# Kernel tuning notes

Measured on AMD Instinct MI355X. Metric: run time of the kernel, lower is better.

Reference implementation:

```python
import jax, jax.numpy as jnp
import numpy as np

S, T, D, H, DQ, F = 2048, 2048, 1024, 16, 1024, 4096
HD = DQ // H


def _layernorm(x, w, b, eps=1e-5):
    mu = jnp.mean(x, axis=-1, keepdims=True)
    var = jnp.mean((x - mu) ** 2, axis=-1, keepdims=True)
    return (x - mu) / jnp.sqrt(var + eps) * w + b


def _attention(q_in, kv_in, mask, wq, bq, wk, bk, wv, bv, wo, bo):
    # q_in: [Sq, D], kv_in: [Sk, D]
    q = (q_in @ wq + bq).reshape(-1, H, HD).transpose(1, 0, 2)   # [H, Sq, hd]
    k = (kv_in @ wk + bk).reshape(-1, H, HD).transpose(1, 0, 2)  # [H, Sk, hd]
    v = (kv_in @ wv + bv).reshape(-1, H, HD).transpose(1, 0, 2)
    scale = jnp.sqrt(jnp.asarray(HD, dtype=q.dtype))
    scores = jnp.einsum('hqd,hkd->hqk', q, k) / scale            # [H, Sq, Sk]
    if mask is not None:
        scores = jnp.where(mask, scores, jnp.finfo(scores.dtype).min)
    attn = jax.nn.softmax(scores, axis=-1)
    ctx = jnp.einsum('hqk,hkd->hqd', attn, v)                    # [H, Sq, hd]
    ctx = ctx.transpose(1, 0, 2).reshape(-1, H * HD)             # [Sq, DQ]
    return ctx @ wo + bo


def setup_inputs() -> dict:
    key = jax.random.key(0)
    ks = jax.random.split(key, 20)

    def lin(kk, fan_in, shape):
        return jax.random.normal(kk, shape, dtype=jnp.float32) / np.sqrt(fan_in)

    inp = {
        'inputs': jax.random.normal(ks[0], (S, D), dtype=jnp.float32),
        'encoder_outputs': jax.random.normal(ks[1], (T, D), dtype=jnp.float32),
        'self_attention_mask': jnp.tril(jnp.ones((S, S), dtype=bool)),
        'cross_attention_mask': jnp.ones((S, T), dtype=bool),
        'ln1_w': jnp.ones((D,), jnp.float32), 'ln1_b': jnp.zeros((D,), jnp.float32),
        'ln2_w': jnp.ones((D,), jnp.float32), 'ln2_b': jnp.zeros((D,), jnp.float32),
        'ln3_w': jnp.ones((D,), jnp.float32), 'ln3_b': jnp.zeros((D,), jnp.float32),
        'sa_wq': lin(ks[2], D, (D, DQ)), 'sa_bq': jnp.zeros((DQ,), jnp.float32),
        'sa_wk': lin(ks[3], D, (D, DQ)), 'sa_bk': jnp.zeros((DQ,), jnp.float32),
        'sa_wv': lin(ks[4], D, (D, DQ)), 'sa_bv': jnp.zeros((DQ,), jnp.float32),
        'sa_wo': lin(ks[5], DQ, (DQ, D)), 'sa_bo': jnp.zeros((D,), jnp.float32),
        'ca_wq': lin(ks[6], D, (D, DQ)), 'ca_bq': jnp.zeros((DQ,), jnp.float32),
        'ca_wk': lin(ks[7], D, (D, DQ)), 'ca_bk': jnp.zeros((DQ,), jnp.float32),
        'ca_wv': lin(ks[8], D, (D, DQ)), 'ca_bv': jnp.zeros((DQ,), jnp.float32),
        'ca_wo': lin(ks[9], DQ, (DQ, D)), 'ca_bo': jnp.zeros((D,), jnp.float32),
        'mlp_wi': lin(ks[10], D, (D, F)), 'mlp_bi': jnp.zeros((F,), jnp.float32),
        'mlp_wo': lin(ks[11], F, (F, D)), 'mlp_bo': jnp.zeros((D,), jnp.float32),
    }
    return inp


def reference(inputs, encoder_outputs, self_attention_mask, cross_attention_mask,
              ln1_w, ln1_b, ln2_w, ln2_b, ln3_w, ln3_b,
              sa_wq, sa_bq, sa_wk, sa_bk, sa_wv, sa_bv, sa_wo, sa_bo,
              ca_wq, ca_bq, ca_wk, ca_bk, ca_wv, ca_bv, ca_wo, ca_bo,
              mlp_wi, mlp_bi, mlp_wo, mlp_bo):
    # pre-norm self-attention
    n1 = _layernorm(inputs, ln1_w, ln1_b)
    x = inputs + _attention(n1, n1, self_attention_mask,
                            sa_wq, sa_bq, sa_wk, sa_bk, sa_wv, sa_bv, sa_wo, sa_bo)
    # pre-norm cross-attention (kv from encoder, not normalized)
    n2 = _layernorm(x, ln2_w, ln2_b)
    x = x + _attention(n2, encoder_outputs, cross_attention_mask,
                       ca_wq, ca_bq, ca_wk, ca_bk, ca_wv, ca_bv, ca_wo, ca_bo)
    # pre-norm MLP
    n3 = _layernorm(x, ln3_w, ln3_b)
    h = jax.nn.relu(n3 @ mlp_wi + mlp_bi)
    return x + (h @ mlp_wo + mlp_bo)
```

## Files before the change

kernel.cpp:

```cpp
#include <hip/hip_runtime.h>


#define S_LEN 2048
#define T_LEN 2048
#define D_DIM 1024
#define H_NUM 16
#define DQ_DIM 1024
#define F_DIM 4096
#define HD_DIM 64

typedef _Float16 f16x8 __attribute__((ext_vector_type(8)));
typedef _Float16 f16x4 __attribute__((ext_vector_type(4)));
typedef float f32x4 __attribute__((ext_vector_type(4)));

__device__ __forceinline__ void split1(float x, _Float16& h, _Float16& l) {
    _Float16 hh = (_Float16)x;
    h = hh;
    l = (_Float16)((x - (float)hh) * 2048.0f);
}

struct WC8 { const float* w[8]; _Float16* th[8]; _Float16* tl[8]; };

__global__ __launch_bounds__(256)
void wconv_kernel(WC8 a, int K, int N) {
    __shared__ __align__(16) _Float16 th[64][72], tl[64][72];
    const float* W = a.w[blockIdx.z];
    _Float16* Th = a.th[blockIdx.z];
    _Float16* Tl = a.tl[blockIdx.z];
    int n0 = blockIdx.x * 64, k0 = blockIdx.y * 64;
    int t = threadIdx.x;
#pragma unroll
    for (int i = 0; i < 4; ++i) {
        int idx = i * 256 + t;
        int kk = idx >> 4, nq = idx & 15;
        float4 w4 = *(const float4*)(W + (size_t)(k0 + kk) * N + n0 + nq * 4);
        _Float16 h, l;
        split1(w4.x, h, l); th[nq * 4 + 0][kk] = h; tl[nq * 4 + 0][kk] = l;
        split1(w4.y, h, l); th[nq * 4 + 1][kk] = h; tl[nq * 4 + 1][kk] = l;
        split1(w4.z, h, l); th[nq * 4 + 2][kk] = h; tl[nq * 4 + 2][kk] = l;
        split1(w4.w, h, l); th[nq * 4 + 3][kk] = h; tl[nq * 4 + 3][kk] = l;
    }
    __syncthreads();
#pragma unroll
    for (int i = 0; i < 2; ++i) {
        int idx = i * 256 + t;
        int nn = idx >> 3, kq = idx & 7;
        *(f16x8*)(Th + (size_t)(n0 + nn) * K + k0 + kq * 8) = *(const f16x8*)&th[nn][kq * 8];
        *(f16x8*)(Tl + (size_t)(n0 + nn) * K + k0 + kq * 8) = *(const f16x8*)&tl[nn][kq * 8];
    }
}

__global__ __launch_bounds__(256)
void esplit_kernel(const float* __restrict__ x, _Float16* __restrict__ hi,
                   _Float16* __restrict__ lo) {
    size_t i = ((size_t)blockIdx.x * 256 + threadIdx.x) * 4;
    float4 v = *(const float4*)(x + i);
    f16x4 hv, lv; _Float16 h, l;
    split1(v.x, h, l); hv[0] = h; lv[0] = l;
    split1(v.y, h, l); hv[1] = h; lv[1] = l;
    split1(v.z, h, l); hv[2] = h; lv[2] = l;
    split1(v.w, h, l); hv[3] = h; lv[3] = l;
    *(f16x4*)(hi + i) = hv;
    *(f16x4*)(lo + i) = lv;
}

__global__ __launch_bounds__(256)
void ln_kernel(const float* __restrict__ x, const float* __restrict__ w,
               const float* __restrict__ b, _Float16* __restrict__ outh,
               _Float16* __restrict__ outl) {
    int row = blockIdx.x;
    int t = threadIdx.x;
    float4 v = ((const float4*)(x + (size_t)row * D_DIM))[t];
    float s = v.x + v.y + v.z + v.w;
    float ss = v.x * v.x + v.y * v.y + v.z * v.z + v.w * v.w;
#pragma unroll
    for (int m = 1; m < 64; m <<= 1) {
        s += __shfl_xor(s, m, 64);
        ss += __shfl_xor(ss, m, 64);
    }
    __shared__ float ps[4], pss[4];
    int wid = t >> 6;
    if ((t & 63) == 0) { ps[wid] = s; pss[wid] = ss; }
    __syncthreads();
    s = ps[0] + ps[1] + ps[2] + ps[3];
    ss = pss[0] + pss[1] + pss[2] + pss[3];
    float mu = s * (1.0f / D_DIM);
    float var = ss * (1.0f / D_DIM) - mu * mu;
    float rstd = rsqrtf(var + 1e-5f);
    float4 wv = ((const float4*)w)[t];
    float4 bv = ((const float4*)b)[t];
    f16x4 hv, lv; _Float16 h, l;
    split1((v.x - mu) * rstd * wv.x + bv.x, h, l); hv[0] = h; lv[0] = l;
    split1((v.y - mu) * rstd * wv.y + bv.y, h, l); hv[1] = h; lv[1] = l;
    split1((v.z - mu) * rstd * wv.z + bv.z, h, l); hv[2] = h; lv[2] = l;
    split1((v.w - mu) * rstd * wv.w + bv.w, h, l); hv[3] = h; lv[3] = l;
    *(f16x4*)(outh + (size_t)row * D_DIM + t * 4) = hv;
    *(f16x4*)(outl + (size_t)row * D_DIM + t * 4) = lv;
}

struct GemmArgs {
    const _Float16 *Ah[3], *Al[3];
    const _Float16 *Bh[3], *Bl[3];
    const float *bias[3];
    void *C0[3];
    void *C1[3];
};

template <int EPI, int BM>
__global__ __launch_bounds__(256, 2)
void gemm_kernel(GemmArgs ga, int M, int N, int K) {
    static_assert(BM == 64 || BM == 128, "BM");
    constexpr int MI = BM / 32;
    constexpr int CA = BM / 32;
    int z = blockIdx.z;
    const _Float16* Ap[2] = {ga.Ah[z], ga.Al[z]};
    const _Float16* Bp[2] = {ga.Bh[z], ga.Bl[z]};
    const float* bias = ga.bias[z];
    void* C0 = ga.C0[z];
    void* C1 = ga.C1[z];

    __shared__ __align__(16) _Float16 sA[2][BM][64];
    __shared__ __align__(16) _Float16 sB[2][64][64];

    int t = threadIdx.x;
    int m0 = blockIdx.y * BM, n0 = blockIdx.x * 64;
    int lane = t & 63, wid = t >> 6;
    int g = lane >> 4, l15 = lane & 15;
    int wm = wid >> 1, wn = wid & 1;

    f32x4 acc1[MI][2] = {};
    f32x4 acc2[MI][2] = {};

    f16x8 ra[2][CA], rb[2][2];
    const int nt = K / 64;

#pragma unroll
    for (int p = 0; p < 2; ++p) {
#pragma unroll
        for (int i = 0; i < CA; ++i) {
            int id = i * 256 + t, row = id >> 3, c = id & 7;
            ra[p][i] = *(const f16x8*)(Ap[p] + (size_t)(m0 + row) * K + c * 8);
        }
#pragma unroll
        for (int i = 0; i < 2; ++i) {
            int id = i * 256 + t, row = id >> 3, c = id & 7;
            rb[p][i] = *(const f16x8*)(Bp[p] + (size_t)(n0 + row) * K + c * 8);
        }
    }

    for (int kt = 0; kt < nt; ++kt) {
        __syncthreads();
#pragma unroll
        for (int p = 0; p < 2; ++p) {
#pragma unroll
            for (int i = 0; i < CA; ++i) {
                int id = i * 256 + t, row = id >> 3, c = id & 7;
                *(f16x8*)&sA[p][row][(c ^ (row & 7)) * 8] = ra[p][i];
            }
#pragma unroll
            for (int i = 0; i < 2; ++i) {
                int id = i * 256 + t, row = id >> 3, c = id & 7;
                *(f16x8*)&sB[p][row][(c ^ (row & 7)) * 8] = rb[p][i];
            }
        }
        if (kt + 1 < nt) {
            int k0 = (kt + 1) * 64;
#pragma unroll
            for (int p = 0; p < 2; ++p) {
#pragma unroll
                for (int i = 0; i < CA; ++i) {
                    int id = i * 256 + t, row = id >> 3, c = id & 7;
                    ra[p][i] = *(const f16x8*)(Ap[p] + (size_t)(m0 + row) * K + k0 + c * 8);
                }
#pragma unroll
                for (int i = 0; i < 2; ++i) {
                    int id = i * 256 + t, row = id >> 3, c = id & 7;
                    rb[p][i] = *(const f16x8*)(Bp[p] + (size_t)(n0 + row) * K + k0 + c * 8);
                }
            }
        }
        __syncthreads();
#pragma unroll
        for (int ks = 0; ks < 2; ++ks) {
            f16x8 ah[MI], al[MI], bh[2], bl[2];
#pragma unroll
            for (int mi = 0; mi < MI; ++mi) {
                int row = wm * (BM / 2) + mi * 16 + l15;
                int cc = ((ks * 4 + g) ^ (row & 7)) * 8;
                ah[mi] = *(const f16x8*)&sA[0][row][cc];
                al[mi] = *(const f16x8*)&sA[1][row][cc];
            }
#pragma unroll
            for (int ni = 0; ni < 2; ++ni) {
                int row = wn * 32 + ni * 16 + l15;
                int cc = ((ks * 4 + g) ^ (row & 7)) * 8;
                bh[ni] = *(const f16x8*)&sB[0][row][cc];
                bl[ni] = *(const f16x8*)&sB[1][row][cc];
            }
#pragma unroll
            for (int mi = 0; mi < MI; ++mi)
#pragma unroll
                for (int ni = 0; ni < 2; ++ni) {
                    acc1[mi][ni] = __builtin_amdgcn_mfma_f32_16x16x32_f16(ah[mi], bh[ni], acc1[mi][ni], 0, 0, 0);
                    acc2[mi][ni] = __builtin_amdgcn_mfma_f32_16x16x32_f16(ah[mi], bl[ni], acc2[mi][ni], 0, 0, 0);
                    acc2[mi][ni] = __builtin_amdgcn_mfma_f32_16x16x32_f16(al[mi], bh[ni], acc2[mi][ni], 0, 0, 0);
                }
        }
    }

#pragma unroll
    for (int ni = 0; ni < 2; ++ni) {
        int col = n0 + wn * 32 + ni * 16 + l15;
        float bb = bias[col];
#pragma unroll
        for (int mi = 0; mi < MI; ++mi) {
#pragma unroll
            for (int r = 0; r < 4; ++r) {
                int row = m0 + wm * (BM / 2) + mi * 16 + g * 4 + r;
                float v = acc1[mi][ni][r] + acc2[mi][ni][r] * (1.0f / 2048.0f) + bb;
                size_t off = (size_t)row * N + col;
                if constexpr (EPI == 0) {
                    ((_Float16*)C0)[off] = (_Float16)v;
                } else if constexpr (EPI == 1) {
                    ((float*)C0)[off] = v + ((const float*)C1)[off];
                } else {
                    _Float16 h, l;
                    split1(fmaxf(v, 0.0f), h, l);
                    ((_Float16*)C0)[off] = h;
                    ((_Float16*)C1)[off] = l;
                }
            }
        }
    }
}

template <bool CAUSAL>
__global__ __launch_bounds__(256)
void flash_kernel(const _Float16* __restrict__ Qm, const _Float16* __restrict__ Km,
                  const _Float16* __restrict__ Vm, _Float16* __restrict__ Oh,
                  _Float16* __restrict__ Ol, int Sk) {
    __shared__ __align__(16) _Float16 sK[64][72];
    __shared__ __align__(16) _Float16 sV[64][72];
    __shared__ __align__(16) _Float16 sP[4][16][72];

    int t = threadIdx.x, lane = t & 63, wid = t >> 6;
    int g = lane >> 4, l15 = lane & 15;
    int qt = blockIdx.x, h = blockIdx.y;
    int q0w = qt * 64 + wid * 16;

    f16x8 aq[2];
    {
        const _Float16* qp = Qm + (size_t)(q0w + l15) * DQ_DIM + h * HD_DIM;
#pragma unroll
        for (int ks = 0; ks < 2; ++ks) {
            f16x8 a = *(const f16x8*)(qp + ks * 32 + g * 8);
#pragma unroll
            for (int e = 0; e < 8; ++e) a[e] = a[e] * (_Float16)0.125f;
            aq[ks] = a;
        }
    }

    float m_old[4] = {-1e30f, -1e30f, -1e30f, -1e30f};
    float l_run[4] = {0.f, 0.f, 0.f, 0.f};
    f32x4 o[4] = {};

    int ntiles = CAUSAL ? (qt + 1) : (Sk / 64);
    for (int jt = 0; jt < ntiles; ++jt) {
        int j0 = jt * 64;
        __syncthreads();
#pragma unroll
        for (int i = 0; i < 2; ++i) {
            int idx = i * 256 + t;
            int jj = idx >> 3, dq = idx & 7;
            *(f16x8*)&sK[jj][dq * 8] =
                *(const f16x8*)(Km + (size_t)(j0 + jj) * DQ_DIM + h * HD_DIM + dq * 8);
            f16x8 v8 = *(const f16x8*)(Vm + (size_t)(j0 + jj) * DQ_DIM + h * HD_DIM + dq * 8);
#pragma unroll
            for (int e = 0; e < 8; ++e) sV[dq * 8 + e][jj] = v8[e];
        }
        __syncthreads();

        f32x4 sc[4] = {};
#pragma unroll
        for (int cf = 0; cf < 4; ++cf)
#pragma unroll
            for (int ks = 0; ks < 2; ++ks) {
                f16x8 bk = *(const f16x8*)&sK[cf * 16 + l15][ks * 32 + g * 8];
                sc[cf] = __builtin_amdgcn_mfma_f32_16x16x32_f16(aq[ks], bk, sc[cf], 0, 0, 0);
            }
        if (CAUSAL && jt == qt) {
#pragma unroll
            for (int cf = 0; cf < 4; ++cf)
#pragma unroll
                for (int r = 0; r < 4; ++r)
                    if (j0 + cf * 16 + l15 > q0w + g * 4 + r) sc[cf][r] = -1e30f;
        }

#pragma unroll
        for (int r = 0; r < 4; ++r) {
            float tmax = fmaxf(fmaxf(sc[0][r], sc[1][r]), fmaxf(sc[2][r], sc[3][r]));
#pragma unroll
            for (int mm = 1; mm < 16; mm <<= 1) tmax = fmaxf(tmax, __shfl_xor(tmax, mm, 64));
            float mn = fmaxf(m_old[r], tmax);
            float corr = __expf(m_old[r] - mn);
            float rs = 0.0f;
#pragma unroll
            for (int cf = 0; cf < 4; ++cf) {
                float p = __expf(sc[cf][r] - mn);
                sc[cf][r] = p;
                rs += p;
            }
#pragma unroll
            for (int mm = 1; mm < 16; mm <<= 1) rs += __shfl_xor(rs, mm, 64);
            l_run[r] = l_run[r] * corr + rs;
            m_old[r] = mn;
#pragma unroll
            for (int hf = 0; hf < 4; ++hf) o[hf][r] *= corr;
        }

#pragma unroll
        for (int cf = 0; cf < 4; ++cf)
#pragma unroll
            for (int r = 0; r < 4; ++r)
                sP[wid][g * 4 + r][cf * 16 + l15] = (_Float16)sc[cf][r];
        __syncthreads();
#pragma unroll
        for (int ks = 0; ks < 2; ++ks) {
            f16x8 ap = *(const f16x8*)&sP[wid][l15][ks * 32 + g * 8];
#pragma unroll
            for (int hf = 0; hf < 4; ++hf) {
                f16x8 bv = *(const f16x8*)&sV[hf * 16 + l15][ks * 32 + g * 8];
                o[hf] = __builtin_amdgcn_mfma_f32_16x16x32_f16(ap, bv, o[hf], 0, 0, 0);
            }
        }
    }

#pragma unroll
    for (int hf = 0; hf < 4; ++hf)
#pragma unroll
        for (int r = 0; r < 4; ++r) {
            int row = q0w + g * 4 + r;
            int col = h * HD_DIM + hf * 16 + l15;
            _Float16 hh, ll;
            split1(o[hf][r] / l_run[r], hh, ll);
            Oh[(size_t)row * DQ_DIM + col] = hh;
            Ol[(size_t)row * DQ_DIM + col] = ll;
        }
}

#define MB(x) ((size_t)(x) * 1024 * 1024)

extern "C" void kernel_launch(void* const* d_in, const int* in_sizes, int n_in,
                              void* d_out, int out_size, void* d_ws, size_t ws_size,
                              hipStream_t stream) {
    const float* x_in = (const float*)d_in[0];
    const float* enc  = (const float*)d_in[1];
    const float* ln1w = (const float*)d_in[4];  const float* ln1b = (const float*)d_in[5];
    const float* ln2w = (const float*)d_in[6];  const float* ln2b = (const float*)d_in[7];
    const float* ln3w = (const float*)d_in[8];  const float* ln3b = (const float*)d_in[9];
    const float* sa_wq = (const float*)d_in[10]; const float* sa_bq = (const float*)d_in[11];
    const float* sa_wk = (const float*)d_in[12]; const float* sa_bk = (const float*)d_in[13];
    const float* sa_wv = (const float*)d_in[14]; const float* sa_bv = (const float*)d_in[15];
    const float* sa_wo = (const float*)d_in[16]; const float* sa_bo = (const float*)d_in[17];
    const float* ca_wq = (const float*)d_in[18]; const float* ca_bq = (const float*)d_in[19];
    const float* ca_wk = (const float*)d_in[20]; const float* ca_bk = (const float*)d_in[21];
    const float* ca_wv = (const float*)d_in[22]; const float* ca_bv = (const float*)d_in[23];
    const float* ca_wo = (const float*)d_in[24]; const float* ca_bo = (const float*)d_in[25];
    const float* mlp_wi = (const float*)d_in[26]; const float* mlp_bi = (const float*)d_in[27];
    const float* mlp_wo = (const float*)d_in[28]; const float* mlp_bo = (const float*)d_in[29];
    float* out = (float*)d_out;

    char* base = (char*)d_ws;
    float* X        = (float*)(base + MB(0));
    _Float16* Nbh   = (_Float16*)(base + MB(8));
    _Float16* Nbl   = (_Float16*)(base + MB(12));
    _Float16* Qb    = (_Float16*)(base + MB(16));
    _Float16* Kb    = (_Float16*)(base + MB(20));
    _Float16* Vb    = (_Float16*)(base + MB(24));
    _Float16* CXh   = (_Float16*)(base + MB(28));
    _Float16* CXl   = (_Float16*)(base + MB(32));
    _Float16* wT[8][2];
    const float* wsrc[8] = {sa_wq, sa_wk, sa_wv, sa_wo, ca_wq, ca_wk, ca_wv, ca_wo};
    for (int i = 0; i < 8; ++i) {
        wT[i][0] = (_Float16*)(base + MB(36 + 4 * i));
        wT[i][1] = (_Float16*)(base + MB(36 + 4 * i) + MB(2));
    }
    _Float16* wiTh  = (_Float16*)(base + MB(68));
    _Float16* wiTl  = (_Float16*)(base + MB(76));
    _Float16* woTh  = (_Float16*)(base + MB(84));
    _Float16* woTl  = (_Float16*)(base + MB(92));
    _Float16* ench  = (_Float16*)(base + MB(100));
    _Float16* encl  = (_Float16*)(base + MB(104));
    _Float16* Hbh   = (_Float16*)(base + MB(36));
    _Float16* Hbl   = (_Float16*)(base + MB(52));

    dim3 blk(256);

    {
        WC8 a;
        for (int i = 0; i < 8; ++i) { a.w[i] = wsrc[i]; a.th[i] = wT[i][0]; a.tl[i] = wT[i][1]; }
        wconv_kernel<<<dim3(16, 16, 8), blk, 0, stream>>>(a, D_DIM, DQ_DIM);
    }
    {
        WC8 a = {};
        a.w[0] = mlp_wi; a.th[0] = wiTh; a.tl[0] = wiTl;
        wconv_kernel<<<dim3(F_DIM / 64, D_DIM / 64, 1), blk, 0, stream>>>(a, D_DIM, F_DIM);
    }
    {
        WC8 a = {};
        a.w[0] = mlp_wo; a.th[0] = woTh; a.tl[0] = woTl;
        wconv_kernel<<<dim3(D_DIM / 64, F_DIM / 64, 1), blk, 0, stream>>>(a, F_DIM, D_DIM);
    }
    esplit_kernel<<<(size_t)T_LEN * D_DIM / 1024, blk, 0, stream>>>(enc, ench, encl);

    ln_kernel<<<S_LEN, blk, 0, stream>>>(x_in, ln1w, ln1b, Nbh, Nbl);
    {
        GemmArgs a = {};
        for (int z = 0; z < 3; ++z) { a.Ah[z] = Nbh; a.Al[z] = Nbl; }
        a.Bh[0] = wT[0][0]; a.Bl[0] = wT[0][1]; a.bias[0] = sa_bq; a.C0[0] = Qb;
        a.Bh[1] = wT[1][0]; a.Bl[1] = wT[1][1]; a.bias[1] = sa_bk; a.C0[1] = Kb;
        a.Bh[2] = wT[2][0]; a.Bl[2] = wT[2][1]; a.bias[2] = sa_bv; a.C0[2] = Vb;
        gemm_kernel<0, 128><<<dim3(DQ_DIM / 64, S_LEN / 128, 3), blk, 0, stream>>>(
            a, S_LEN, DQ_DIM, D_DIM);
    }
    flash_kernel<true><<<dim3(S_LEN / 64, H_NUM), blk, 0, stream>>>(Qb, Kb, Vb, CXh, CXl, S_LEN);
    {
        GemmArgs a = {};
        a.Ah[0] = CXh; a.Al[0] = CXl;
        a.Bh[0] = wT[3][0]; a.Bl[0] = wT[3][1]; a.bias[0] = sa_bo;
        a.C0[0] = X; a.C1[0] = (void*)x_in;
        gemm_kernel<1, 64><<<dim3(D_DIM / 64, S_LEN / 64, 1), blk, 0, stream>>>(
            a, S_LEN, D_DIM, DQ_DIM);
    }

    ln_kernel<<<S_LEN, blk, 0, stream>>>(X, ln2w, ln2b, Nbh, Nbl);
    {
        GemmArgs a = {};
        a.Ah[0] = Nbh;  a.Al[0] = Nbl;
        a.Ah[1] = ench; a.Al[1] = encl;
        a.Ah[2] = ench; a.Al[2] = encl;
        a.Bh[0] = wT[4][0]; a.Bl[0] = wT[4][1]; a.bias[0] = ca_bq; a.C0[0] = Qb;
        a.Bh[1] = wT[5][0]; a.Bl[1] = wT[5][1]; a.bias[1] = ca_bk; a.C0[1] = Kb;
        a.Bh[2] = wT[6][0]; a.Bl[2] = wT[6][1]; a.bias[2] = ca_bv; a.C0[2] = Vb;
        gemm_kernel<0, 128><<<dim3(DQ_DIM / 64, S_LEN / 128, 3), blk, 0, stream>>>(
            a, S_LEN, DQ_DIM, D_DIM);
    }
    flash_kernel<false><<<dim3(S_LEN / 64, H_NUM), blk, 0, stream>>>(Qb, Kb, Vb, CXh, CXl, T_LEN);
    {
        GemmArgs a = {};
        a.Ah[0] = CXh; a.Al[0] = CXl;
        a.Bh[0] = wT[7][0]; a.Bl[0] = wT[7][1]; a.bias[0] = ca_bo;
        a.C0[0] = X; a.C1[0] = X;
        gemm_kernel<1, 64><<<dim3(D_DIM / 64, S_LEN / 64, 1), blk, 0, stream>>>(
            a, S_LEN, D_DIM, DQ_DIM);
    }

    ln_kernel<<<S_LEN, blk, 0, stream>>>(X, ln3w, ln3b, Nbh, Nbl);
    {
        GemmArgs a = {};
        a.Ah[0] = Nbh; a.Al[0] = Nbl;
        a.Bh[0] = wiTh; a.Bl[0] = wiTl; a.bias[0] = mlp_bi;
        a.C0[0] = Hbh; a.C1[0] = Hbl;
        gemm_kernel<2, 128><<<dim3(F_DIM / 64, S_LEN / 128, 1), blk, 0, stream>>>(
            a, S_LEN, F_DIM, D_DIM);
    }
    {
        GemmArgs a = {};
        a.Ah[0] = Hbh; a.Al[0] = Hbl;
        a.Bh[0] = woTh; a.Bl[0] = woTl; a.bias[0] = mlp_bo;
        a.C0[0] = out; a.C1[0] = X;
        gemm_kernel<1, 64><<<dim3(D_DIM / 64, S_LEN / 64, 1), blk, 0, stream>>>(
            a, S_LEN, D_DIM, F_DIM);
    }

    (void)in_sizes; (void)n_in; (void)out_size; (void)ws_size;
}
```

Measured before the change: 688.2 us.

## Use direct global-to-LDS loads in GEMM, transposed V output, paired-tile flash attention

```diff
diff --git a/kernel.cpp b/kernel.cpp
--- a/kernel.cpp
+++ b/kernel.cpp
@@ -17,6 +17,12 @@
     _Float16 hh = (_Float16)x;
     h = hh;
     l = (_Float16)((x - (float)hh) * 2048.0f);
+}
+
+__device__ __forceinline__ void gload16(const void* g, void* l) {
+    __builtin_amdgcn_global_load_lds(
+        (const __attribute__((address_space(1))) void*)g,
+        (__attribute__((address_space(3))) void*)l, 16, 0, 0);
 }
 
 struct WC8 { const float* w[8]; _Float16* th[8]; _Float16* tl[8]; };
@@ -104,6 +110,7 @@
     const float *bias[3];
     void *C0[3];
     void *C1[3];
+    int trans[3];
 };
 
 template <int EPI, int BM>
@@ -111,16 +118,19 @@
 void gemm_kernel(GemmArgs ga, int M, int N, int K) {
     static_assert(BM == 64 || BM == 128, "BM");
     constexpr int MI = BM / 32;
-    constexpr int CA = BM / 32;
+    constexpr int ASZ = BM * 32;
+    constexpr int BUFSZ = 2 * ASZ + 4096;
     int z = blockIdx.z;
-    const _Float16* Ap[2] = {ga.Ah[z], ga.Al[z]};
-    const _Float16* Bp[2] = {ga.Bh[z], ga.Bl[z]};
+    const _Float16* Ah = ga.Ah[z];
+    const _Float16* Al = ga.Al[z];
+    const _Float16* Bh = ga.Bh[z];
+    const _Float16* Bl = ga.Bl[z];
     const float* bias = ga.bias[z];
     void* C0 = ga.C0[z];
     void* C1 = ga.C1[z];
-
-    __shared__ __align__(16) _Float16 sA[2][BM][64];
-    __shared__ __align__(16) _Float16 sB[2][64][64];
+    int tr = ga.trans[z];
+
+    __shared__ __align__(16) _Float16 lds[2 * BUFSZ];
 
     int t = threadIdx.x;
     int m0 = blockIdx.y * BM, n0 = blockIdx.x * 64;
@@ -131,81 +141,56 @@
     f32x4 acc1[MI][2] = {};
     f32x4 acc2[MI][2] = {};
 
-    f16x8 ra[2][CA], rb[2][2];
-    const int nt = K / 64;
-
-#pragma unroll
-    for (int p = 0; p < 2; ++p) {
-#pragma unroll
-        for (int i = 0; i < CA; ++i) {
-            int id = i * 256 + t, row = id >> 3, c = id & 7;
-            ra[p][i] = *(const f16x8*)(Ap[p] + (size_t)(m0 + row) * K + c * 8);
-        }
-#pragma unroll
-        for (int i = 0; i < 2; ++i) {
-            int id = i * 256 + t, row = id >> 3, c = id & 7;
-            rb[p][i] = *(const f16x8*)(Bp[p] + (size_t)(n0 + row) * K + c * 8);
-        }
-    }
-
+    const int nt = K / 32;
+
+    auto stage = [&](int kt, int bi) {
+        int k0 = kt * 32;
+        _Float16* buf = &lds[bi * BUFSZ];
+#pragma unroll
+        for (int c = 0; c < BM / 64; ++c) {
+            int chunk = c * 256 + t;
+            int row = chunk >> 2, cc = chunk & 3;
+            int so = k0 + ((cc ^ (row & 3)) << 3);
+            gload16(Ah + (size_t)(m0 + row) * K + so, buf + chunk * 8);
+            gload16(Al + (size_t)(m0 + row) * K + so, buf + ASZ + chunk * 8);
+        }
+        {
+            int chunk = t;
+            int row = chunk >> 2, cc = chunk & 3;
+            int so = k0 + ((cc ^ (row & 3)) << 3);
+            gload16(Bh + (size_t)(n0 + row) * K + so, buf + 2 * ASZ + chunk * 8);
+            gload16(Bl + (size_t)(n0 + row) * K + so, buf + 2 * ASZ + 2048 + chunk * 8);
+        }
+    };
+
+    stage(0, 0);
     for (int kt = 0; kt < nt; ++kt) {
         __syncthreads();
-#pragma unroll
-        for (int p = 0; p < 2; ++p) {
-#pragma unroll
-            for (int i = 0; i < CA; ++i) {
-                int id = i * 256 + t, row = id >> 3, c = id & 7;
-                *(f16x8*)&sA[p][row][(c ^ (row & 7)) * 8] = ra[p][i];
+        if (kt + 1 < nt) stage(kt + 1, (kt + 1) & 1);
+        const _Float16* buf = &lds[(kt & 1) * BUFSZ];
+        f16x8 ah[MI], al[MI], bh[2], bl[2];
+#pragma unroll
+        for (int mi = 0; mi < MI; ++mi) {
+            int row = wm * (BM / 2) + mi * 16 + l15;
+            int cof = row * 32 + ((g ^ (row & 3)) << 3);
+            ah[mi] = *(const f16x8*)&buf[cof];
+            al[mi] = *(const f16x8*)&buf[ASZ + cof];
+        }
+#pragma unroll
+        for (int ni = 0; ni < 2; ++ni) {
+            int row = wn * 32 + ni * 16 + l15;
+            int cof = row * 32 + ((g ^ (row & 3)) << 3);
+            bh[ni] = *(const f16x8*)&buf[2 * ASZ + cof];
+            bl[ni] = *(const f16x8*)&buf[2 * ASZ + 2048 + cof];
+        }
+#pragma unroll
+        for (int mi = 0; mi < MI; ++mi)
+#pragma unroll
+            for (int ni = 0; ni < 2; ++ni) {
+                acc1[mi][ni] = __builtin_amdgcn_mfma_f32_16x16x32_f16(ah[mi], bh[ni], acc1[mi][ni], 0, 0, 0);
+                acc2[mi][ni] = __builtin_amdgcn_mfma_f32_16x16x32_f16(ah[mi], bl[ni], acc2[mi][ni], 0, 0, 0);
+                acc2[mi][ni] = __builtin_amdgcn_mfma_f32_16x16x32_f16(al[mi], bh[ni], acc2[mi][ni], 0, 0, 0);
             }
-#pragma unroll
-            for (int i = 0; i < 2; ++i) {
-                int id = i * 256 + t, row = id >> 3, c = id & 7;
-                *(f16x8*)&sB[p][row][(c ^ (row & 7)) * 8] = rb[p][i];
-            }
-        }
-        if (kt + 1 < nt) {
-            int k0 = (kt + 1) * 64;
-#pragma unroll
-            for (int p = 0; p < 2; ++p) {
-#pragma unroll
-                for (int i = 0; i < CA; ++i) {
-                    int id = i * 256 + t, row = id >> 3, c = id & 7;
-                    ra[p][i] = *(const f16x8*)(Ap[p] + (size_t)(m0 + row) * K + k0 + c * 8);
-                }
-#pragma unroll
-                for (int i = 0; i < 2; ++i) {
-                    int id = i * 256 + t, row = id >> 3, c = id & 7;
-                    rb[p][i] = *(const f16x8*)(Bp[p] + (size_t)(n0 + row) * K + k0 + c * 8);
-                }
-            }
-        }
-        __syncthreads();
-#pragma unroll
-        for (int ks = 0; ks < 2; ++ks) {
-            f16x8 ah[MI], al[MI], bh[2], bl[2];
-#pragma unroll
-            for (int mi = 0; mi < MI; ++mi) {
-                int row = wm * (BM / 2) + mi * 16 + l15;
-                int cc = ((ks * 4 + g) ^ (row & 7)) * 8;
-                ah[mi] = *(const f16x8*)&sA[0][row][cc];
-                al[mi] = *(const f16x8*)&sA[1][row][cc];
-            }
-#pragma unroll
-            for (int ni = 0; ni < 2; ++ni) {
-                int row = wn * 32 + ni * 16 + l15;
-                int cc = ((ks * 4 + g) ^ (row & 7)) * 8;
-                bh[ni] = *(const f16x8*)&sB[0][row][cc];
-                bl[ni] = *(const f16x8*)&sB[1][row][cc];
-            }
-#pragma unroll
-            for (int mi = 0; mi < MI; ++mi)
-#pragma unroll
-                for (int ni = 0; ni < 2; ++ni) {
-                    acc1[mi][ni] = __builtin_amdgcn_mfma_f32_16x16x32_f16(ah[mi], bh[ni], acc1[mi][ni], 0, 0, 0);
-                    acc2[mi][ni] = __builtin_amdgcn_mfma_f32_16x16x32_f16(ah[mi], bl[ni], acc2[mi][ni], 0, 0, 0);
-                    acc2[mi][ni] = __builtin_amdgcn_mfma_f32_16x16x32_f16(al[mi], bh[ni], acc2[mi][ni], 0, 0, 0);
-                }
-        }
     }
 
 #pragma unroll
@@ -214,18 +199,34 @@
         float bb = bias[col];
 #pragma unroll
         for (int mi = 0; mi < MI; ++mi) {
-#pragma unroll
-            for (int r = 0; r < 4; ++r) {
-                int row = m0 + wm * (BM / 2) + mi * 16 + g * 4 + r;
-                float v = acc1[mi][ni][r] + acc2[mi][ni][r] * (1.0f / 2048.0f) + bb;
-                size_t off = (size_t)row * N + col;
-                if constexpr (EPI == 0) {
-                    ((_Float16*)C0)[off] = (_Float16)v;
-                } else if constexpr (EPI == 1) {
-                    ((float*)C0)[off] = v + ((const float*)C1)[off];
+            int row0 = m0 + wm * (BM / 2) + mi * 16 + g * 4;
+            float vr[4];
+#pragma unroll
+            for (int r = 0; r < 4; ++r)
+                vr[r] = acc1[mi][ni][r] + acc2[mi][ni][r] * (1.0f / 2048.0f) + bb;
+            if constexpr (EPI == 0) {
+                if (tr) {
+                    f16x4 tv;
+#pragma unroll
+                    for (int r = 0; r < 4; ++r) tv[r] = (_Float16)vr[r];
+                    *(f16x4*)((_Float16*)C0 + (size_t)col * M + row0) = tv;
                 } else {
+#pragma unroll
+                    for (int r = 0; r < 4; ++r)
+                        ((_Float16*)C0)[(size_t)(row0 + r) * N + col] = (_Float16)vr[r];
+                }
+            } else if constexpr (EPI == 1) {
+#pragma unroll
+                for (int r = 0; r < 4; ++r) {
+                    size_t off = (size_t)(row0 + r) * N + col;
+                    ((float*)C0)[off] = vr[r] + ((const float*)C1)[off];
+                }
+            } else {
+#pragma unroll
+                for (int r = 0; r < 4; ++r) {
+                    size_t off = (size_t)(row0 + r) * N + col;
                     _Float16 h, l;
-                    split1(fmaxf(v, 0.0f), h, l);
+                    split1(fmaxf(vr[r], 0.0f), h, l);
                     ((_Float16*)C0)[off] = h;
                     ((_Float16*)C1)[off] = l;
                 }
@@ -237,19 +238,20 @@
 template <bool CAUSAL>
 __global__ __launch_bounds__(256)
 void flash_kernel(const _Float16* __restrict__ Qm, const _Float16* __restrict__ Km,
-                  const _Float16* __restrict__ Vm, _Float16* __restrict__ Oh,
+                  const _Float16* __restrict__ VT, _Float16* __restrict__ Oh,
                   _Float16* __restrict__ Ol, int Sk) {
     __shared__ __align__(16) _Float16 sK[64][72];
-    __shared__ __align__(16) _Float16 sV[64][72];
+    __shared__ __align__(16) _Float16 sVT[64][72];
     __shared__ __align__(16) _Float16 sP[4][16][72];
 
     int t = threadIdx.x, lane = t & 63, wid = t >> 6;
     int g = lane >> 4, l15 = lane & 15;
-    int qt = blockIdx.x, h = blockIdx.y;
-    int q0w = qt * 64 + wid * 16;
-
-    f16x8 aq[2];
-    {
+    int h = blockIdx.y;
+    int NT = Sk / 64;
+    int ta = blockIdx.x, tb = NT - 1 - ta;
+    int q0A = ta * 64 + wid * 16, q0B = tb * 64 + wid * 16;
+
+    auto loadQ = [&](int q0w, f16x8* aq) {
         const _Float16* qp = Qm + (size_t)(q0w + l15) * DQ_DIM + h * HD_DIM;
 #pragma unroll
         for (int ks = 0; ks < 2; ++ks) {
@@ -258,28 +260,30 @@
             for (int e = 0; e < 8; ++e) a[e] = a[e] * (_Float16)0.125f;
             aq[ks] = a;
         }
-    }
-
-    float m_old[4] = {-1e30f, -1e30f, -1e30f, -1e30f};
-    float l_run[4] = {0.f, 0.f, 0.f, 0.f};
-    f32x4 o[4] = {};
-
-    int ntiles = CAUSAL ? (qt + 1) : (Sk / 64);
-    for (int jt = 0; jt < ntiles; ++jt) {
+    };
+    f16x8 aqA[2], aqB[2];
+    loadQ(q0A, aqA);
+    loadQ(q0B, aqB);
+
+    float mA[4], lA[4], mB[4], lB[4];
+    f32x4 oA[4] = {}, oB[4] = {};
+#pragma unroll
+    for (int r = 0; r < 4; ++r) { mA[r] = mB[r] = -1e30f; lA[r] = lB[r] = 0.f; }
+
+    f16x8 rk[2], rv[2];
+    auto loadKV = [&](int jt) {
         int j0 = jt * 64;
-        __syncthreads();
 #pragma unroll
         for (int i = 0; i < 2; ++i) {
-            int idx = i * 256 + t;
-            int jj = idx >> 3, dq = idx & 7;
-            *(f16x8*)&sK[jj][dq * 8] =
-                *(const f16x8*)(Km + (size_t)(j0 + jj) * DQ_DIM + h * HD_DIM + dq * 8);
-            f16x8 v8 = *(const f16x8*)(Vm + (size_t)(j0 + jj) * DQ_DIM + h * HD_DIM + dq * 8);
-#pragma unroll
-            for (int e = 0; e < 8; ++e) sV[dq * 8 + e][jj] = v8[e];
-        }
-        __syncthreads();
-
+            int id = i * 256 + t, r_ = id >> 3, c = id & 7;
+            rk[i] = *(const f16x8*)(Km + (size_t)(j0 + r_) * DQ_DIM + h * HD_DIM + c * 8);
+            rv[i] = *(const f16x8*)(VT + (size_t)(h * HD_DIM + r_) * Sk + j0 + c * 8);
+        }
+    };
+
+    auto doTile = [&](const f16x8* aq, int q0w, int tidx, float* m_, float* l_,
+                      f32x4* o, int jt) {
+        int j0 = jt * 64;
         f32x4 sc[4] = {};
 #pragma unroll
         for (int cf = 0; cf < 4; ++cf)
@@ -288,21 +292,20 @@
                 f16x8 bk = *(const f16x8*)&sK[cf * 16 + l15][ks * 32 + g * 8];
                 sc[cf] = __builtin_amdgcn_mfma_f32_16x16x32_f16(aq[ks], bk, sc[cf], 0, 0, 0);
             }
-        if (CAUSAL && jt == qt) {
+        if (CAUSAL && jt == tidx) {
 #pragma unroll
             for (int cf = 0; cf < 4; ++cf)
 #pragma unroll
                 for (int r = 0; r < 4; ++r)
                     if (j0 + cf * 16 + l15 > q0w + g * 4 + r) sc[cf][r] = -1e30f;
         }
-
 #pragma unroll
         for (int r = 0; r < 4; ++r) {
             float tmax = fmaxf(fmaxf(sc[0][r], sc[1][r]), fmaxf(sc[2][r], sc[3][r]));
 #pragma unroll
             for (int mm = 1; mm < 16; mm <<= 1) tmax = fmaxf(tmax, __shfl_xor(tmax, mm, 64));
-            float mn = fmaxf(m_old[r], tmax);
-            float corr = __expf(m_old[r] - mn);
+            float mn = fmaxf(m_[r], tmax);
+            float corr = __expf(m_[r] - mn);
             float rs = 0.0f;
 #pragma unroll
             for (int cf = 0; cf < 4; ++cf) {
@@ -312,40 +315,58 @@
             }
 #pragma unroll
             for (int mm = 1; mm < 16; mm <<= 1) rs += __shfl_xor(rs, mm, 64);
-            l_run[r] = l_run[r] * corr + rs;
-            m_old[r] = mn;
+            l_[r] = l_[r] * corr + rs;
+            m_[r] = mn;
 #pragma unroll
             for (int hf = 0; hf < 4; ++hf) o[hf][r] *= corr;
         }
-
 #pragma unroll
         for (int cf = 0; cf < 4; ++cf)
 #pragma unroll
             for (int r = 0; r < 4; ++r)
                 sP[wid][g * 4 + r][cf * 16 + l15] = (_Float16)sc[cf][r];
-        __syncthreads();
 #pragma unroll
         for (int ks = 0; ks < 2; ++ks) {
             f16x8 ap = *(const f16x8*)&sP[wid][l15][ks * 32 + g * 8];
 #pragma unroll
             for (int hf = 0; hf < 4; ++hf) {
-                f16x8 bv = *(const f16x8*)&sV[hf * 16 + l15][ks * 32 + g * 8];
+                f16x8 bv = *(const f16x8*)&sVT[hf * 16 + l15][ks * 32 + g * 8];
                 o[hf] = __builtin_amdgcn_mfma_f32_16x16x32_f16(ap, bv, o[hf], 0, 0, 0);
             }
         }
-    }
-
-#pragma unroll
-    for (int hf = 0; hf < 4; ++hf)
-#pragma unroll
-        for (int r = 0; r < 4; ++r) {
-            int row = q0w + g * 4 + r;
-            int col = h * HD_DIM + hf * 16 + l15;
-            _Float16 hh, ll;
-            split1(o[hf][r] / l_run[r], hh, ll);
-            Oh[(size_t)row * DQ_DIM + col] = hh;
-            Ol[(size_t)row * DQ_DIM + col] = ll;
-        }
+    };
+
+    loadKV(0);
+    int jend = CAUSAL ? tb : NT - 1;
+    for (int jt = 0; jt <= jend; ++jt) {
+        __syncthreads();
+#pragma unroll
+        for (int i = 0; i < 2; ++i) {
+            int id = i * 256 + t, r_ = id >> 3, c = id & 7;
+            *(f16x8*)&sK[r_][c * 8] = rk[i];
+            *(f16x8*)&sVT[r_][c * 8] = rv[i];
+        }
+        if (jt < jend) loadKV(jt + 1);
+        __syncthreads();
+        doTile(aqB, q0B, tb, mB, lB, oB, jt);
+        if (!CAUSAL || jt <= ta) doTile(aqA, q0A, ta, mA, lA, oA, jt);
+    }
+
+    auto writeO = [&](int q0w, float* l_, f32x4* o) {
+#pragma unroll
+        for (int hf = 0; hf < 4; ++hf)
+#pragma unroll
+            for (int r = 0; r < 4; ++r) {
+                int row = q0w + g * 4 + r;
+                int col = h * HD_DIM + hf * 16 + l15;
+                _Float16 hh, ll;
+                split1(o[hf][r] / l_[r], hh, ll);
+                Oh[(size_t)row * DQ_DIM + col] = hh;
+                Ol[(size_t)row * DQ_DIM + col] = ll;
+            }
+    };
+    writeO(q0A, lA, oA);
+    writeO(q0B, lB, oB);
 }
 
 #define MB(x) ((size_t)(x) * 1024 * 1024)
@@ -376,7 +397,7 @@
     _Float16* Nbl   = (_Float16*)(base + MB(12));
     _Float16* Qb    = (_Float16*)(base + MB(16));
     _Float16* Kb    = (_Float16*)(base + MB(20));
-    _Float16* Vb    = (_Float16*)(base + MB(24));
+    _Float16* VTb   = (_Float16*)(base + MB(24));
     _Float16* CXh   = (_Float16*)(base + MB(28));
     _Float16* CXl   = (_Float16*)(base + MB(32));
     _Float16* wT[8][2];
@@ -419,11 +440,12 @@
         for (int z = 0; z < 3; ++z) { a.Ah[z] = Nbh; a.Al[z] = Nbl; }
         a.Bh[0] = wT[0][0]; a.Bl[0] = wT[0][1]; a.bias[0] = sa_bq; a.C0[0] = Qb;
         a.Bh[1] = wT[1][0]; a.Bl[1] = wT[1][1]; a.bias[1] = sa_bk; a.C0[1] = Kb;
-        a.Bh[2] = wT[2][0]; a.Bl[2] = wT[2][1]; a.bias[2] = sa_bv; a.C0[2] = Vb;
+        a.Bh[2] = wT[2][0]; a.Bl[2] = wT[2][1]; a.bias[2] = sa_bv; a.C0[2] = VTb;
+        a.trans[2] = 1;
         gemm_kernel<0, 128><<<dim3(DQ_DIM / 64, S_LEN / 128, 3), blk, 0, stream>>>(
             a, S_LEN, DQ_DIM, D_DIM);
     }
-    flash_kernel<true><<<dim3(S_LEN / 64, H_NUM), blk, 0, stream>>>(Qb, Kb, Vb, CXh, CXl, S_LEN);
+    flash_kernel<true><<<dim3(S_LEN / 128, H_NUM), blk, 0, stream>>>(Qb, Kb, VTb, CXh, CXl, S_LEN);
     {
         GemmArgs a = {};
         a.Ah[0] = CXh; a.Al[0] = CXl;
@@ -441,11 +463,12 @@
         a.Ah[2] = ench; a.Al[2] = encl;
         a.Bh[0] = wT[4][0]; a.Bl[0] = wT[4][1]; a.bias[0] = ca_bq; a.C0[0] = Qb;
         a.Bh[1] = wT[5][0]; a.Bl[1] = wT[5][1]; a.bias[1] = ca_bk; a.C0[1] = Kb;
-        a.Bh[2] = wT[6][0]; a.Bl[2] = wT[6][1]; a.bias[2] = ca_bv; a.C0[2] = Vb;
+        a.Bh[2] = wT[6][0]; a.Bl[2] = wT[6][1]; a.bias[2] = ca_bv; a.C0[2] = VTb;
+        a.trans[2] = 1;
         gemm_kernel<0, 128><<<dim3(DQ_DIM / 64, S_LEN / 128, 3), blk, 0, stream>>>(
             a, S_LEN, DQ_DIM, D_DIM);
     }
-    flash_kernel<false><<<dim3(S_LEN / 64, H_NUM), blk, 0, stream>>>(Qb, Kb, Vb, CXh, CXl, T_LEN);
+    flash_kernel<false><<<dim3(S_LEN / 128, H_NUM), blk, 0, stream>>>(Qb, Kb, VTb, CXh, CXl, T_LEN);
     {
         GemmArgs a = {};
         a.Ah[0] = CXh; a.Al[0] = CXl;
```

Result: faster. 608.4 us (-11.6%).
